# Optimization experiments

Measured on AMD Instinct MI355X. Metric: run time of the kernel, lower is better.

The kernel has to match this reference:

```python
import jax, jax.numpy as jnp
import numpy as np

B, S_IMG, S_TXT, D, H, HD = 1, 4096, 512, 3072, 24, 128
EPS = 1e-5
SCALE = 1.0 / np.sqrt(HD)


def _linear(x, W, b=None):
    # torch nn.Linear: y = x @ W.T + b, W is [out, in]
    y = jnp.einsum('bsd,od->bso', x, W)
    return y if b is None else y + b


def _rmsnorm(x, w):
    # over last dim (head_dim), torch nn.RMSNorm with affine weight
    var = jnp.mean(jnp.square(x), axis=-1, keepdims=True)
    return x * jax.lax.rsqrt(var + EPS) * w


def _rope(x, cos, sin):
    # x: [B, S, H, D]; cos/sin: [S, D]; interleaved-pair rotation
    xr = x.reshape(*x.shape[:-1], HD // 2, 2)
    x_real, x_imag = xr[..., 0], xr[..., 1]
    x_rot = jnp.stack([-x_imag, x_real], axis=-1).reshape(x.shape)
    return x * cos[None, :, None, :] + x_rot * sin[None, :, None, :]


def setup_inputs() -> dict:
    key = jax.random.key(0)
    ks = jax.random.split(key, 24)
    s = 0.02
    inp = {
        'hidden_states': jax.random.normal(ks[0], (B, S_IMG, D), jnp.float32),
        'encoder_hidden_states': jax.random.normal(ks[1], (B, S_TXT, D), jnp.float32),
        'rope_cos': jax.random.uniform(ks[2], (S_IMG + S_TXT, HD), jnp.float32),
        'rope_sin': jax.random.uniform(ks[3], (S_IMG + S_TXT, HD), jnp.float32),
        # image-stream qkv (bias=False)
        'Wq': jax.random.normal(ks[4], (D, D), jnp.float32) * s,
        'Wk': jax.random.normal(ks[5], (D, D), jnp.float32) * s,
        'Wv': jax.random.normal(ks[6], (D, D), jnp.float32) * s,
        # text-stream qkv (bias=True)
        'Waq': jax.random.normal(ks[7], (D, D), jnp.float32) * s,
        'baq': jnp.zeros((D,), jnp.float32),
        'Wak': jax.random.normal(ks[8], (D, D), jnp.float32) * s,
        'bak': jnp.zeros((D,), jnp.float32),
        'Wav': jax.random.normal(ks[9], (D, D), jnp.float32) * s,
        'bav': jnp.zeros((D,), jnp.float32),
        # output projections (bias=True)
        'Wo': jax.random.normal(ks[10], (D, D), jnp.float32) * s,
        'bo': jnp.zeros((D,), jnp.float32),
        'Wao': jax.random.normal(ks[11], (D, D), jnp.float32) * s,
        'bao': jnp.zeros((D,), jnp.float32),
        # RMSNorm weights on head_dim
        'wq_norm': jnp.ones((HD,), jnp.float32),
        'wk_norm': jnp.ones((HD,), jnp.float32),
        'waq_norm': jnp.ones((HD,), jnp.float32),
        'wak_norm': jnp.ones((HD,), jnp.float32),
    }
    return inp


def reference(hidden_states, encoder_hidden_states, rope_cos, rope_sin,
              Wq, Wk, Wv, Waq, baq, Wak, bak, Wav, bav,
              Wo, bo, Wao, bao, wq_norm, wk_norm, waq_norm, wak_norm):
    # image-stream qkv -> [B, S_img, H, HD]
    q = _linear(hidden_states, Wq).reshape(B, S_IMG, H, HD)
    k = _linear(hidden_states, Wk).reshape(B, S_IMG, H, HD)
    v = _linear(hidden_states, Wv).reshape(B, S_IMG, H, HD)
    q = _rmsnorm(q, wq_norm)
    k = _rmsnorm(k, wk_norm)
    # text-stream qkv -> [B, S_txt, H, HD]
    eq = _linear(encoder_hidden_states, Waq, baq).reshape(B, S_TXT, H, HD)
    ek = _linear(encoder_hidden_states, Wak, bak).reshape(B, S_TXT, H, HD)
    ev = _linear(encoder_hidden_states, Wav, bav).reshape(B, S_TXT, H, HD)
    eq = _rmsnorm(eq, waq_norm)
    ek = _rmsnorm(ek, wak_norm)
    # concat [encoder, image] along sequence
    q = jnp.concatenate([eq, q], axis=1)  # [B, S_total, H, HD]
    k = jnp.concatenate([ek, k], axis=1)
    v = jnp.concatenate([ev, v], axis=1)
    # RoPE on joint sequence
    q = _rope(q, rope_cos, rope_sin)
    k = _rope(k, rope_cos, rope_sin)
    # SDPA over joint sequence
    scores = jnp.einsum('bqhd,bkhd->bhqk', q, k) * SCALE
    probs = jax.nn.softmax(scores, axis=-1)
    out = jnp.einsum('bhqk,bkhd->bqhd', probs, v)  # [B, S_total, H, HD]
    out = out.reshape(B, S_IMG + S_TXT, D)
    enc_out = _linear(out[:, :S_TXT], Wao, bao)
    img_out = _linear(out[:, S_TXT:], Wo, bo)
    return (img_out, enc_out)
```

## Files before the change

kernel.cpp:

```cpp
#include <hip/hip_runtime.h>

typedef __bf16 bf16_t;
typedef __bf16 bf16x8 __attribute__((ext_vector_type(8)));
typedef float  f32x4  __attribute__((ext_vector_type(4)));

#define S_IMG 4096
#define S_TXT 512
#define S_TOT 4608
#define DMODEL 3072
#define NH 24
#define HD 128

__device__ __forceinline__ void load_lds16(const void* g, void* l) {
  __builtin_amdgcn_global_load_lds(
      (const __attribute__((address_space(1))) void*)g,
      (__attribute__((address_space(3))) void*)l, 16, 0, 0);
}

#define BARRIER() do { asm volatile("" ::: "memory");                          \
                       __builtin_amdgcn_s_barrier();                           \
                       asm volatile("" ::: "memory"); } while (0)

__global__ __launch_bounds__(256) void f2b_kernel(const float* __restrict__ in,
                                                  bf16_t* __restrict__ out, int n) {
  int i = (blockIdx.x * 256 + threadIdx.x) * 4;
  if (i >= n) return;
  float4 v = *(const float4*)(in + i);
  union { bf16_t b[4]; uint2 u; } pk;
  pk.b[0] = (bf16_t)v.x; pk.b[1] = (bf16_t)v.y;
  pk.b[2] = (bf16_t)v.z; pk.b[3] = (bf16_t)v.w;
  *(uint2*)(out + i) = pk.u;
}

__global__ __launch_bounds__(256) void f2b2_kernel(
    const float* __restrict__ in0, bf16_t* __restrict__ out0,
    const float* __restrict__ in1, bf16_t* __restrict__ out1, int nb) {
  int b = blockIdx.x;
  const float* in = (b < nb) ? in0 : in1;
  bf16_t* out = (b < nb) ? out0 : out1;
  int i = (((b < nb) ? b : b - nb) * 256 + threadIdx.x) * 4;
  float4 v = *(const float4*)(in + i);
  union { bf16_t b[4]; uint2 u; } pk;
  pk.b[0] = (bf16_t)v.x; pk.b[1] = (bf16_t)v.y;
  pk.b[2] = (bf16_t)v.z; pk.b[3] = (bf16_t)v.w;
  *(uint2*)(out + i) = pk.u;
}

template <typename OT>
__global__ __launch_bounds__(512, 2) void gemm256(
    const bf16_t* __restrict__ A0, const bf16_t* __restrict__ B0,
    OT* __restrict__ C0, const float* __restrict__ bias0, int mt0,
    const bf16_t* __restrict__ A1, const bf16_t* __restrict__ B1,
    OT* __restrict__ C1, const float* __restrict__ bias1, int swzq)
{
  const int NT = DMODEL / 64;
  __shared__ bf16_t As[2][2][256 * 32];
  __shared__ bf16_t Bs[2][2][256 * 32];

  int bid = blockIdx.x;
  int t = (bid & 7) * swzq + (bid >> 3);
  int nb0 = mt0 * 12;
  const bf16_t* A; const bf16_t* B; OT* C; const float* bias;
  if (t < nb0) { A = A0; B = B0; C = C0; bias = bias0; }
  else { t -= nb0; A = A1; B = B1; C = C1; bias = bias1; }
  int bx = t % 12, by = t / 12;

  int tid = threadIdx.x;
  int lane = tid & 63, wid = tid >> 6;
  int l15 = lane & 15, lg = lane >> 4;
  int wm = wid >> 2, wn = wid & 3;
  int sx = (lg ^ ((l15 >> 1) & 3)) * 8;

  const bf16_t* Ag = A + (size_t)by * 256 * DMODEL;
  const bf16_t* Bg = B + (size_t)bx * 256 * DMODEL;

  int ur0 = tid >> 2;
  int uc0 = ((tid & 3) ^ ((tid >> 3) & 3)) * 8;

  auto stage = [&](int ht) {
    int T = ht >> 2, sl = ht & 3, kh = sl >> 1;
    const bf16_t* G = (sl & 1) ? Bg : Ag;
    bf16_t* L = (sl & 1) ? &Bs[T & 1][kh][0] : &As[T & 1][kh][0];
    int kbase = T * 64 + kh * 32;
    #pragma unroll
    for (int j = 0; j < 2; j++) {
      int r = j * 128 + ur0;
      load_lds16(G + (size_t)r * DMODEL + kbase + uc0,
                 (char*)L + (size_t)(j * 512 + tid) * 16);
    }
  };

  f32x4 acc[8][4];
  f32x4 zero = {0.f, 0.f, 0.f, 0.f};
  #pragma unroll
  for (int m = 0; m < 8; m++)
    #pragma unroll
    for (int n = 0; n < 4; n++) acc[m][n] = zero;

  stage(0); stage(1); stage(2); stage(3); stage(4); stage(5);
  asm volatile("s_waitcnt vmcnt(8)" ::: "memory");
  BARRIER();

  for (int T = 0; T < NT; ++T) {
    int cur = T & 1;
    const bf16_t* A0s = &As[cur][0][0];
    const bf16_t* A1s = &As[cur][1][0];
    const bf16_t* B0s = &Bs[cur][0][0];
    const bf16_t* B1s = &Bs[cur][1][0];
    bf16x8 af[4], bfr[4];

    #pragma unroll
    for (int n = 0; n < 4; n++)
      bfr[n] = *(const bf16x8*)(B0s + (wn * 64 + n * 16 + l15) * 32 + sx);
    #pragma unroll
    for (int m = 0; m < 4; m++)
      af[m] = *(const bf16x8*)(A0s + (wm * 128 + m * 16 + l15) * 32 + sx);
    if (T + 1 < NT) stage(4 * T + 6);
    BARRIER();
    __builtin_amdgcn_s_setprio(1);
    #pragma unroll
    for (int m = 0; m < 4; m++)
      #pragma unroll
      for (int n = 0; n < 4; n++)
        acc[m][n] = __builtin_amdgcn_mfma_f32_16x16x32_bf16(af[m], bfr[n], acc[m][n], 0, 0, 0);
    __builtin_amdgcn_s_setprio(0);
    BARRIER();

    #pragma unroll
    for (int m = 0; m < 4; m++)
      af[m] = *(const bf16x8*)(A0s + (wm * 128 + 64 + m * 16 + l15) * 32 + sx);
    if (T + 1 < NT) stage(4 * T + 7);
    BARRIER();
    __builtin_amdgcn_s_setprio(1);
    #pragma unroll
    for (int m = 0; m < 4; m++)
      #pragma unroll
      for (int n = 0; n < 4; n++)
        acc[4 + m][n] = __builtin_amdgcn_mfma_f32_16x16x32_bf16(af[m], bfr[n], acc[4 + m][n], 0, 0, 0);
    __builtin_amdgcn_s_setprio(0);
    if (T < NT - 1) asm volatile("s_waitcnt vmcnt(8)" ::: "memory");
    else            asm volatile("s_waitcnt vmcnt(0)" ::: "memory");
    BARRIER();

    #pragma unroll
    for (int n = 0; n < 4; n++)
      bfr[n] = *(const bf16x8*)(B1s + (wn * 64 + n * 16 + l15) * 32 + sx);
    #pragma unroll
    for (int m = 0; m < 4; m++)
      af[m] = *(const bf16x8*)(A1s + (wm * 128 + m * 16 + l15) * 32 + sx);
    if (T + 2 < NT) stage(4 * T + 8);
    BARRIER();
    __builtin_amdgcn_s_setprio(1);
    #pragma unroll
    for (int m = 0; m < 4; m++)
      #pragma unroll
      for (int n = 0; n < 4; n++)
        acc[m][n] = __builtin_amdgcn_mfma_f32_16x16x32_bf16(af[m], bfr[n], acc[m][n], 0, 0, 0);
    __builtin_amdgcn_s_setprio(0);
    BARRIER();

    #pragma unroll
    for (int m = 0; m < 4; m++)
      af[m] = *(const bf16x8*)(A1s + (wm * 128 + 64 + m * 16 + l15) * 32 + sx);
    if (T + 2 < NT) stage(4 * T + 9);
    BARRIER();
    __builtin_amdgcn_s_setprio(1);
    #pragma unroll
    for (int m = 0; m < 4; m++)
      #pragma unroll
      for (int n = 0; n < 4; n++)
        acc[4 + m][n] = __builtin_amdgcn_mfma_f32_16x16x32_bf16(af[m], bfr[n], acc[4 + m][n], 0, 0, 0);
    __builtin_amdgcn_s_setprio(0);
    if (T < NT - 2)       asm volatile("s_waitcnt vmcnt(8)" ::: "memory");
    else if (T == NT - 2) asm volatile("s_waitcnt vmcnt(4)" ::: "memory");
    BARRIER();
  }

  size_t row0 = (size_t)by * 256 + wm * 128;
  int col0 = bx * 256 + wn * 64;
  #pragma unroll
  for (int n = 0; n < 4; n++) {
    int col = col0 + n * 16 + l15;
    float bv = bias ? bias[col] : 0.f;
    #pragma unroll
    for (int m = 0; m < 8; m++) {
      #pragma unroll
      for (int r = 0; r < 4; r++) {
        size_t row = row0 + m * 16 + lg * 4 + r;
        C[row * DMODEL + col] = (OT)(acc[m][n][r] + bv);
      }
    }
  }
}

template <typename OT>
__global__ __launch_bounds__(1024) void gemm1024(
    const bf16_t* __restrict__ A0, const bf16_t* __restrict__ B0,
    OT* __restrict__ C0, const float* __restrict__ bias0, int mt0,
    const bf16_t* __restrict__ A1, const bf16_t* __restrict__ B1,
    OT* __restrict__ C1, const float* __restrict__ bias1, int swzq)
{
  const int NT = DMODEL / 64;
  __shared__ bf16_t As[2][2][256 * 32];
  __shared__ bf16_t Bs[2][2][256 * 32];

  int bid = blockIdx.x;
  int t = (bid & 7) * swzq + (bid >> 3);
  int nb0 = mt0 * 12;
  const bf16_t* A; const bf16_t* B; OT* C; const float* bias;
  if (t < nb0) { A = A0; B = B0; C = C0; bias = bias0; }
  else { t -= nb0; A = A1; B = B1; C = C1; bias = bias1; }
  int bx = t % 12, by = t / 12;

  int tid = threadIdx.x;
  int lane = tid & 63, wid = tid >> 6;
  int l15 = lane & 15, lg = lane >> 4;
  int wm = wid >> 2, wn = wid & 3;
  int sx = (lg ^ ((l15 >> 1) & 3)) * 8;

  const bf16_t* Ag = A + (size_t)by * 256 * DMODEL;
  const bf16_t* Bg = B + (size_t)bx * 256 * DMODEL;

  int ur0 = tid >> 2;
  int uc0 = ((tid & 3) ^ ((tid >> 3) & 3)) * 8;

  auto stage = [&](int ht) {
    int T = ht >> 2, sl = ht & 3, kh = sl >> 1;
    const bf16_t* G = (sl & 1) ? Bg : Ag;
    bf16_t* L = (sl & 1) ? &Bs[T & 1][kh][0] : &As[T & 1][kh][0];
    int kbase = T * 64 + kh * 32;
    load_lds16(G + (size_t)ur0 * DMODEL + kbase + uc0,
               (char*)L + (size_t)tid * 16);
  };

  f32x4 acc[4][4];
  f32x4 zero = {0.f, 0.f, 0.f, 0.f};
  #pragma unroll
  for (int m = 0; m < 4; m++)
    #pragma unroll
    for (int n = 0; n < 4; n++) acc[m][n] = zero;

  stage(0); stage(1); stage(2); stage(3); stage(4); stage(5);
  asm volatile("s_waitcnt vmcnt(4)" ::: "memory");
  BARRIER();

  for (int T = 0; T < NT; ++T) {
    int cur = T & 1;
    bf16x8 af[4], bfr[4];

    {
      const bf16_t* A0s = &As[cur][0][0];
      const bf16_t* B0s = &Bs[cur][0][0];
      #pragma unroll
      for (int n = 0; n < 4; n++)
        bfr[n] = *(const bf16x8*)(B0s + (wn * 64 + n * 16 + l15) * 32 + sx);
      #pragma unroll
      for (int m = 0; m < 4; m++)
        af[m] = *(const bf16x8*)(A0s + (wm * 64 + m * 16 + l15) * 32 + sx);
    }
    if (T + 1 < NT) { stage(4 * T + 6); stage(4 * T + 7); }
    BARRIER();
    __builtin_amdgcn_s_setprio(1);
    #pragma unroll
    for (int m = 0; m < 4; m++)
      #pragma unroll
      for (int n = 0; n < 4; n++)
        acc[m][n] = __builtin_amdgcn_mfma_f32_16x16x32_bf16(af[m], bfr[n], acc[m][n], 0, 0, 0);
    __builtin_amdgcn_s_setprio(0);
    if (T < NT - 1) asm volatile("s_waitcnt vmcnt(4)" ::: "memory");
    else            asm volatile("s_waitcnt vmcnt(0)" ::: "memory");
    BARRIER();

    {
      const bf16_t* A1s = &As[cur][1][0];
      const bf16_t* B1s = &Bs[cur][1][0];
      #pragma unroll
      for (int n = 0; n < 4; n++)
        bfr[n] = *(const bf16x8*)(B1s + (wn * 64 + n * 16 + l15) * 32 + sx);
      #pragma unroll
      for (int m = 0; m < 4; m++)
        af[m] = *(const bf16x8*)(A1s + (wm * 64 + m * 16 + l15) * 32 + sx);
    }
    if (T + 2 < NT) { stage(4 * T + 8); stage(4 * T + 9); }
    BARRIER();
    __builtin_amdgcn_s_setprio(1);
    #pragma unroll
    for (int m = 0; m < 4; m++)
      #pragma unroll
      for (int n = 0; n < 4; n++)
        acc[m][n] = __builtin_amdgcn_mfma_f32_16x16x32_bf16(af[m], bfr[n], acc[m][n], 0, 0, 0);
    __builtin_amdgcn_s_setprio(0);
    if (T < NT - 2)       asm volatile("s_waitcnt vmcnt(4)" ::: "memory");
    else if (T == NT - 2) asm volatile("s_waitcnt vmcnt(2)" ::: "memory");
    BARRIER();
  }

  size_t row0 = (size_t)by * 256 + wm * 64;
  int col0 = bx * 256 + wn * 64;
  #pragma unroll
  for (int n = 0; n < 4; n++) {
    int col = col0 + n * 16 + l15;
    float bv = bias ? bias[col] : 0.f;
    #pragma unroll
    for (int m = 0; m < 4; m++) {
      #pragma unroll
      for (int r = 0; r < 4; r++) {
        size_t row = row0 + m * 16 + lg * 4 + r;
        C[row * DMODEL + col] = (OT)(acc[m][n][r] + bv);
      }
    }
  }
}

__global__ __launch_bounds__(256) void qk_post(
    const bf16_t* __restrict__ qbuf, const bf16_t* __restrict__ kbuf,
    const float* __restrict__ cosb, const float* __restrict__ sinb,
    const float* __restrict__ wqn, const float* __restrict__ wkn,
    const float* __restrict__ waqn, const float* __restrict__ wakn,
    bf16_t* __restrict__ Qh, bf16_t* __restrict__ Kh)
{
  int gw = blockIdx.x * 4 + (threadIdx.x >> 6);
  int lane = threadIdx.x & 63;
  int s = gw / NH, h = gw - (gw / NH) * NH;
  if (s >= S_TOT) return;
  int d0 = lane * 2;
  const bf16_t* qp = qbuf + (size_t)s * DMODEL + h * HD + d0;
  const bf16_t* kp = kbuf + (size_t)s * DMODEL + h * HD + d0;
  float q0 = (float)qp[0], q1 = (float)qp[1];
  float k0 = (float)kp[0], k1 = (float)kp[1];
  float sq = q0 * q0 + q1 * q1, sk = k0 * k0 + k1 * k1;
  #pragma unroll
  for (int m = 1; m < 64; m <<= 1) { sq += __shfl_xor(sq, m); sk += __shfl_xor(sk, m); }
  float rq = rsqrtf(sq * (1.f / HD) + 1e-5f);
  float rk = rsqrtf(sk * (1.f / HD) + 1e-5f);
  const float* qn = (s < S_TXT) ? waqn : wqn;
  const float* kn = (s < S_TXT) ? wakn : wkn;
  q0 *= rq * qn[d0]; q1 *= rq * qn[d0 + 1];
  k0 *= rk * kn[d0]; k1 *= rk * kn[d0 + 1];
  float c0 = cosb[s * HD + d0], c1 = cosb[s * HD + d0 + 1];
  float s0 = sinb[s * HD + d0], s1 = sinb[s * HD + d0 + 1];
  const float SCALE = 0.1275174319942397f;
  float oq0 = (q0 * c0 - q1 * s0) * SCALE;
  float oq1 = (q1 * c1 + q0 * s1) * SCALE;
  float ok0 = k0 * c0 - k1 * s0;
  float ok1 = k1 * c1 + k0 * s1;
  size_t ob = ((size_t)h * S_TOT + s) * HD + d0;
  union { bf16_t b[2]; unsigned int u; } pq, pk;
  pq.b[0] = (bf16_t)oq0; pq.b[1] = (bf16_t)oq1;
  pk.b[0] = (bf16_t)ok0; pk.b[1] = (bf16_t)ok1;
  *(unsigned int*)(Qh + ob) = pq.u;
  *(unsigned int*)(Kh + ob) = pk.u;
}

__global__ __launch_bounds__(256) void v_trans(const bf16_t* __restrict__ vbuf,
                                               bf16_t* __restrict__ Vt) {
  __shared__ bf16_t tile[64 * 130];
  int h = blockIdx.y, s0 = blockIdx.x * 64;
  int tid = threadIdx.x;
  #pragma unroll
  for (int i = 0; i < 16; i++) {
    int idx = tid + i * 256;
    int sr = idx >> 6, dp = idx & 63;
    unsigned int u = *(const unsigned int*)(vbuf + (size_t)(s0 + sr) * DMODEL + h * HD + dp * 2);
    *(unsigned int*)&tile[sr * 130 + dp * 2] = u;
  }
  __syncthreads();
  #pragma unroll
  for (int i = 0; i < 16; i++) {
    int idx = tid + i * 256;
    int d = idx >> 5, scp = idx & 31;
    union { bf16_t b[2]; unsigned int u; } pk;
    pk.b[0] = tile[(scp * 2) * 130 + d];
    pk.b[1] = tile[(scp * 2 + 1) * 130 + d];
    *(unsigned int*)(Vt + ((size_t)h * HD + d) * S_TOT + s0 + scp * 2) = pk.u;
  }
}

__global__ __launch_bounds__(256, 2) void attn_kernel(
    const bf16_t* __restrict__ Qh, const bf16_t* __restrict__ Kh,
    const bf16_t* __restrict__ Vt, bf16_t* __restrict__ O)
{
  int bid = blockIdx.x;
  int orig = (bid & 7) * 108 + (bid >> 3);
  int h = orig / 36;
  int q0 = (orig % 36) * 128;

  int tid = threadIdx.x, w = tid >> 6, lane = tid & 63;
  int l15 = lane & 15, lg = lane >> 4;
  int sw = (l15 & 7) << 4;

  __shared__ bf16_t Ks[2][64 * 128];
  __shared__ bf16_t Vs[2][128 * 64];
  __shared__ bf16_t Ps[4][32 * 64];

  const bf16_t* Kbase = Kh + (size_t)h * S_TOT * HD;
  const bf16_t* Vbase = Vt + (size_t)h * HD * S_TOT;
  bf16_t* Pw = &Ps[w][0];

  bf16x8 qf[2][4];
  #pragma unroll
  for (int qh = 0; qh < 2; qh++) {
    const bf16_t* Qrow = Qh + ((size_t)h * S_TOT + q0 + w * 32 + qh * 16 + l15) * HD + lg * 8;
    #pragma unroll
    for (int dc = 0; dc < 4; dc++) qf[qh][dc] = *(const bf16x8*)(Qrow + dc * 32);
  }

  f32x4 o[2][8];
  f32x4 zero = {0.f, 0.f, 0.f, 0.f};
  #pragma unroll
  for (int qh = 0; qh < 2; qh++)
    #pragma unroll
    for (int i = 0; i < 8; i++) o[qh][i] = zero;
  float m0 = -1e30f, m1 = -1e30f, l0 = 0.f, l1 = 0.f;

#define STAGE(buf, kt) do {                                                    \
    _Pragma("unroll")                                                          \
    for (int i_ = 0; i_ < 4; i_++) {                                           \
      int Lb = (tid + i_ * 256) * 16; int row = Lb >> 8, cb = Lb & 255;        \
      int sb = cb ^ ((row & 7) << 4);                                          \
      load_lds16(Kbase + (size_t)((kt) + row) * HD + (sb >> 1),                \
                 (char*)Ks[buf] + Lb);                                         \
    }                                                                          \
    _Pragma("unroll")                                                          \
    for (int i_ = 0; i_ < 4; i_++) {                                           \
      int Lb = (tid + i_ * 256) * 16; int row = Lb >> 7, cb = Lb & 127;        \
      int sb = cb ^ ((row & 7) << 4);                                          \
      load_lds16(Vbase + (size_t)row * S_TOT + (kt) + (sb >> 1),               \
                 (char*)Vs[buf] + Lb);                                         \
    }                                                                          \
  } while (0)

#define BODY(CUR) do {                                                         \
    f32x4 sacc[2][4];                                                          \
    _Pragma("unroll")                                                          \
    for (int qh = 0; qh < 2; qh++)                                             \
      _Pragma("unroll")                                                        \
      for (int c = 0; c < 4; c++) sacc[qh][c] = zero;                          \
    const char* Kc = (const char*)Ks[CUR];                                     \
    _Pragma("unroll")                                                          \
    for (int c = 0; c < 4; c++) {                                              \
      int row = c * 16 + l15;                                                  \
      int rs = (row & 7) << 4;                                                 \
      const char* kr = Kc + row * 256;                                         \
      _Pragma("unroll")                                                        \
      for (int dc = 0; dc < 4; dc++) {                                         \
        bf16x8 kf = *(const bf16x8*)(kr + ((dc * 64 + lg * 16) ^ rs));         \
        sacc[0][c] = __builtin_amdgcn_mfma_f32_16x16x32_bf16(kf, qf[0][dc], sacc[0][c], 0, 0, 0); \
        sacc[1][c] = __builtin_amdgcn_mfma_f32_16x16x32_bf16(kf, qf[1][dc], sacc[1][c], 0, 0, 0); \
      }                                                                        \
    }                                                                          \
    float px0 = sacc[0][0][0], px1 = sacc[1][0][0];                            \
    _Pragma("unroll")                                                          \
    for (int c = 0; c < 4; c++)                                                \
      _Pragma("unroll")                                                        \
      for (int r = 0; r < 4; r++) {                                            \
        px0 = fmaxf(px0, sacc[0][c][r]);                                       \
        px1 = fmaxf(px1, sacc[1][c][r]);                                       \
      }                                                                        \
    px0 = fmaxf(px0, __shfl_xor(px0, 16)); px0 = fmaxf(px0, __shfl_xor(px0, 32)); \
    px1 = fmaxf(px1, __shfl_xor(px1, 16)); px1 = fmaxf(px1, __shfl_xor(px1, 32)); \
    bool need = (px0 > m0 + 8.f) || (px1 > m1 + 8.f);                          \
    if (__any(need)) {                                                         \
      float mn0 = fmaxf(m0, px0), mn1 = fmaxf(m1, px1);                        \
      float a0 = exp2f(m0 - mn0), a1 = exp2f(m1 - mn1);                        \
      m0 = mn0; m1 = mn1; l0 *= a0; l1 *= a1;                                  \
      _Pragma("unroll")                                                        \
      for (int r = 0; r < 4; r++) {                                            \
        float f0 = __shfl(a0, lg * 4 + r);                                     \
        float f1 = __shfl(a1, lg * 4 + r);                                     \
        _Pragma("unroll")                                                      \
        for (int dn = 0; dn < 8; dn++) { o[0][dn][r] *= f0; o[1][dn][r] *= f1; } \
      }                                                                        \
    }                                                                          \
    _Pragma("unroll")                                                          \
    for (int qh = 0; qh < 2; qh++) {                                           \
      float m = qh ? m1 : m0;                                                  \
      float rsum = 0.f;                                                        \
      char* Prow = (char*)Pw + (qh * 16 + l15) * 128;                          \
      _Pragma("unroll")                                                        \
      for (int c = 0; c < 4; c++) {                                            \
        union { bf16_t b[4]; uint2 u; } pk;                                    \
        _Pragma("unroll")                                                      \
        for (int r = 0; r < 4; r++) {                                          \
          float p = exp2f(sacc[qh][c][r] - m);                                 \
          rsum += p;                                                           \
          pk.b[r] = (bf16_t)p;                                                 \
        }                                                                      \
        *(uint2*)(Prow + ((c * 32 + lg * 8) ^ sw)) = pk.u;                     \
      }                                                                        \
      rsum += __shfl_xor(rsum, 16);                                            \
      rsum += __shfl_xor(rsum, 32);                                            \
      if (qh) l1 += rsum; else l0 += rsum;                                     \
    }                                                                          \
    bf16x8 pf[2][2];                                                           \
    _Pragma("unroll")                                                          \
    for (int qh = 0; qh < 2; qh++) {                                           \
      const char* Prow = (const char*)Pw + (qh * 16 + l15) * 128;              \
      _Pragma("unroll")                                                        \
      for (int kc = 0; kc < 2; kc++)                                           \
        pf[qh][kc] = *(const bf16x8*)(Prow + ((kc * 64 + lg * 16) ^ sw));      \
    }                                                                          \
    const char* Vc = (const char*)Vs[CUR];                                     \
    _Pragma("unroll")                                                          \
    for (int dn = 0; dn < 8; dn++) {                                           \
      int row = dn * 16 + l15;                                                 \
      int rs2 = (row & 7) << 4;                                                \
      const char* vr = Vc + row * 128;                                         \
      bf16x8 vf0 = *(const bf16x8*)(vr + ((lg * 16) ^ rs2));                   \
      bf16x8 vf1 = *(const bf16x8*)(vr + ((64 + lg * 16) ^ rs2));              \
      o[0][dn] = __builtin_amdgcn_mfma_f32_16x16x32_bf16(pf[0][0], vf0, o[0][dn], 0, 0, 0); \
      o[0][dn] = __builtin_amdgcn_mfma_f32_16x16x32_bf16(pf[0][1], vf1, o[0][dn], 0, 0, 0); \
      o[1][dn] = __builtin_amdgcn_mfma_f32_16x16x32_bf16(pf[1][0], vf0, o[1][dn], 0, 0, 0); \
      o[1][dn] = __builtin_amdgcn_mfma_f32_16x16x32_bf16(pf[1][1], vf1, o[1][dn], 0, 0, 0); \
    }                                                                          \
  } while (0)

  STAGE(0, 0);
  __syncthreads();

  const int NT = S_TOT / 64;
  for (int tt = 0; tt < NT; tt += 2) {
    STAGE(1, (tt + 1) * 64);
    BODY(0);
    __syncthreads();
    if (tt + 2 < NT) STAGE(0, (tt + 2) * 64);
    BODY(1);
    __syncthreads();
  }
#undef BODY
#undef STAGE

  #pragma unroll
  for (int qh = 0; qh < 2; qh++) {
    #pragma unroll
    for (int r = 0; r < 4; r++) {
      float lv = __shfl(qh ? l1 : l0, lg * 4 + r);
      float inv = 1.f / lv;
      size_t srow = (size_t)q0 + w * 32 + qh * 16 + lg * 4 + r;
      #pragma unroll
      for (int dn = 0; dn < 8; dn++)
        O[srow * DMODEL + h * HD + dn * 16 + l15] = (bf16_t)(o[qh][dn][r] * inv);
    }
  }
}

extern "C" void kernel_launch(void* const* d_in, const int* in_sizes, int n_in,
                              void* d_out, int out_size, void* d_ws, size_t ws_size,
                              hipStream_t stream) {
  const float* hidden = (const float*)d_in[0];
  const float* enc    = (const float*)d_in[1];
  const float* ropec  = (const float*)d_in[2];
  const float* ropes  = (const float*)d_in[3];
  const float* Wq  = (const float*)d_in[4];
  const float* Wk  = (const float*)d_in[5];
  const float* Wv  = (const float*)d_in[6];
  const float* Waq = (const float*)d_in[7];
  const float* baq = (const float*)d_in[8];
  const float* Wak = (const float*)d_in[9];
  const float* bak = (const float*)d_in[10];
  const float* Wav = (const float*)d_in[11];
  const float* bav = (const float*)d_in[12];
  const float* Wo  = (const float*)d_in[13];
  const float* bo  = (const float*)d_in[14];
  const float* Wao = (const float*)d_in[15];
  const float* bao = (const float*)d_in[16];
  const float* wqn = (const float*)d_in[17];
  const float* wkn = (const float*)d_in[18];
  const float* waqn = (const float*)d_in[19];
  const float* wakn = (const float*)d_in[20];

  const size_t WSZ = (size_t)DMODEL * DMODEL;
  const size_t SEQSZ = (size_t)S_TOT * DMODEL;
  if (ws_size < (2 * WSZ + 6 * SEQSZ) * sizeof(bf16_t)) return;

  bf16_t* s0   = (bf16_t*)d_ws;
  bf16_t* s1   = s0 + WSZ;
  bf16_t* xbi  = s1 + WSZ;
  bf16_t* xbt  = xbi + (size_t)S_IMG * DMODEL;
  bf16_t* qbuf = xbi + SEQSZ;
  bf16_t* kbuf = qbuf + SEQSZ;
  bf16_t* vbuf = kbuf + SEQSZ;
  bf16_t* Kh   = vbuf + SEQSZ;
  bf16_t* Vh   = Kh + SEQSZ;
  bf16_t* Qh   = xbi;
  bf16_t* attn_o = qbuf;
  float* outf = (float*)d_out;

  f2b_kernel<<<S_IMG * DMODEL / 1024, 256, 0, stream>>>(hidden, xbi, S_IMG * DMODEL);
  f2b_kernel<<<S_TXT * DMODEL / 1024, 256, 0, stream>>>(enc, xbt, S_TXT * DMODEL);

  const int WB = (int)(WSZ / 1024);
  f2b2_kernel<<<2 * WB, 256, 0, stream>>>(Wq, s0, Waq, s1, WB);
  gemm1024<bf16_t><<<216, 1024, 0, stream>>>(
      xbi, s0, qbuf + (size_t)S_TXT * DMODEL, nullptr, 16,
      xbt, s1, qbuf, baq, 27);
  f2b2_kernel<<<2 * WB, 256, 0, stream>>>(Wk, s0, Wak, s1, WB);
  gemm256<bf16_t><<<216, 512, 0, stream>>>(
      xbi, s0, kbuf + (size_t)S_TXT * DMODEL, nullptr, 16,
      xbt, s1, kbuf, bak, 27);
  f2b2_kernel<<<2 * WB, 256, 0, stream>>>(Wv, s0, Wav, s1, WB);
  gemm256<bf16_t><<<216, 512, 0, stream>>>(
      xbi, s0, vbuf + (size_t)S_TXT * DMODEL, nullptr, 16,
      xbt, s1, vbuf, bav, 27);

  qk_post<<<S_TOT * NH / 4, 256, 0, stream>>>(qbuf, kbuf, ropec, ropes,
                                              wqn, wkn, waqn, wakn, Qh, Kh);
  v_trans<<<dim3(S_TOT / 64, NH), 256, 0, stream>>>(vbuf, Vh);

  attn_kernel<<<36 * 24, 256, 0, stream>>>(Qh, Kh, Vh, attn_o);

  f2b2_kernel<<<2 * WB, 256, 0, stream>>>(Wo, s0, Wao, s1, WB);
  gemm256<float><<<216, 512, 0, stream>>>(
      attn_o + (size_t)S_TXT * DMODEL, s0, outf, bo, 16,
      attn_o, s1, outf + (size_t)S_IMG * DMODEL, bao, 27);
}
```

Baseline: 938.5 us.

## Fuse V transpose into V-projection GEMM epilogue and use 1024-thread GEMMs

```diff
diff --git a/kernel.cpp b/kernel.cpp
--- a/kernel.cpp
+++ b/kernel.cpp
@@ -47,153 +47,6 @@
 }
 
 template <typename OT>
-__global__ __launch_bounds__(512, 2) void gemm256(
-    const bf16_t* __restrict__ A0, const bf16_t* __restrict__ B0,
-    OT* __restrict__ C0, const float* __restrict__ bias0, int mt0,
-    const bf16_t* __restrict__ A1, const bf16_t* __restrict__ B1,
-    OT* __restrict__ C1, const float* __restrict__ bias1, int swzq)
-{
-  const int NT = DMODEL / 64;
-  __shared__ bf16_t As[2][2][256 * 32];
-  __shared__ bf16_t Bs[2][2][256 * 32];
-
-  int bid = blockIdx.x;
-  int t = (bid & 7) * swzq + (bid >> 3);
-  int nb0 = mt0 * 12;
-  const bf16_t* A; const bf16_t* B; OT* C; const float* bias;
-  if (t < nb0) { A = A0; B = B0; C = C0; bias = bias0; }
-  else { t -= nb0; A = A1; B = B1; C = C1; bias = bias1; }
-  int bx = t % 12, by = t / 12;
-
-  int tid = threadIdx.x;
-  int lane = tid & 63, wid = tid >> 6;
-  int l15 = lane & 15, lg = lane >> 4;
-  int wm = wid >> 2, wn = wid & 3;
-  int sx = (lg ^ ((l15 >> 1) & 3)) * 8;
-
-  const bf16_t* Ag = A + (size_t)by * 256 * DMODEL;
-  const bf16_t* Bg = B + (size_t)bx * 256 * DMODEL;
-
-  int ur0 = tid >> 2;
-  int uc0 = ((tid & 3) ^ ((tid >> 3) & 3)) * 8;
-
-  auto stage = [&](int ht) {
-    int T = ht >> 2, sl = ht & 3, kh = sl >> 1;
-    const bf16_t* G = (sl & 1) ? Bg : Ag;
-    bf16_t* L = (sl & 1) ? &Bs[T & 1][kh][0] : &As[T & 1][kh][0];
-    int kbase = T * 64 + kh * 32;
-    #pragma unroll
-    for (int j = 0; j < 2; j++) {
-      int r = j * 128 + ur0;
-      load_lds16(G + (size_t)r * DMODEL + kbase + uc0,
-                 (char*)L + (size_t)(j * 512 + tid) * 16);
-    }
-  };
-
-  f32x4 acc[8][4];
-  f32x4 zero = {0.f, 0.f, 0.f, 0.f};
-  #pragma unroll
-  for (int m = 0; m < 8; m++)
-    #pragma unroll
-    for (int n = 0; n < 4; n++) acc[m][n] = zero;
-
-  stage(0); stage(1); stage(2); stage(3); stage(4); stage(5);
-  asm volatile("s_waitcnt vmcnt(8)" ::: "memory");
-  BARRIER();
-
-  for (int T = 0; T < NT; ++T) {
-    int cur = T & 1;
-    const bf16_t* A0s = &As[cur][0][0];
-    const bf16_t* A1s = &As[cur][1][0];
-    const bf16_t* B0s = &Bs[cur][0][0];
-    const bf16_t* B1s = &Bs[cur][1][0];
-    bf16x8 af[4], bfr[4];
-
-    #pragma unroll
-    for (int n = 0; n < 4; n++)
-      bfr[n] = *(const bf16x8*)(B0s + (wn * 64 + n * 16 + l15) * 32 + sx);
-    #pragma unroll
-    for (int m = 0; m < 4; m++)
-      af[m] = *(const bf16x8*)(A0s + (wm * 128 + m * 16 + l15) * 32 + sx);
-    if (T + 1 < NT) stage(4 * T + 6);
-    BARRIER();
-    __builtin_amdgcn_s_setprio(1);
-    #pragma unroll
-    for (int m = 0; m < 4; m++)
-      #pragma unroll
-      for (int n = 0; n < 4; n++)
-        acc[m][n] = __builtin_amdgcn_mfma_f32_16x16x32_bf16(af[m], bfr[n], acc[m][n], 0, 0, 0);
-    __builtin_amdgcn_s_setprio(0);
-    BARRIER();
-
-    #pragma unroll
-    for (int m = 0; m < 4; m++)
-      af[m] = *(const bf16x8*)(A0s + (wm * 128 + 64 + m * 16 + l15) * 32 + sx);
-    if (T + 1 < NT) stage(4 * T + 7);
-    BARRIER();
-    __builtin_amdgcn_s_setprio(1);
-    #pragma unroll
-    for (int m = 0; m < 4; m++)
-      #pragma unroll
-      for (int n = 0; n < 4; n++)
-        acc[4 + m][n] = __builtin_amdgcn_mfma_f32_16x16x32_bf16(af[m], bfr[n], acc[4 + m][n], 0, 0, 0);
-    __builtin_amdgcn_s_setprio(0);
-    if (T < NT - 1) asm volatile("s_waitcnt vmcnt(8)" ::: "memory");
-    else            asm volatile("s_waitcnt vmcnt(0)" ::: "memory");
-    BARRIER();
-
-    #pragma unroll
-    for (int n = 0; n < 4; n++)
-      bfr[n] = *(const bf16x8*)(B1s + (wn * 64 + n * 16 + l15) * 32 + sx);
-    #pragma unroll
-    for (int m = 0; m < 4; m++)
-      af[m] = *(const bf16x8*)(A1s + (wm * 128 + m * 16 + l15) * 32 + sx);
-    if (T + 2 < NT) stage(4 * T + 8);
-    BARRIER();
-    __builtin_amdgcn_s_setprio(1);
-    #pragma unroll
-    for (int m = 0; m < 4; m++)
-      #pragma unroll
-      for (int n = 0; n < 4; n++)
-        acc[m][n] = __builtin_amdgcn_mfma_f32_16x16x32_bf16(af[m], bfr[n], acc[m][n], 0, 0, 0);
-    __builtin_amdgcn_s_setprio(0);
-    BARRIER();
-
-    #pragma unroll
-    for (int m = 0; m < 4; m++)
-      af[m] = *(const bf16x8*)(A1s + (wm * 128 + 64 + m * 16 + l15) * 32 + sx);
-    if (T + 2 < NT) stage(4 * T + 9);
-    BARRIER();
-    __builtin_amdgcn_s_setprio(1);
-    #pragma unroll
-    for (int m = 0; m < 4; m++)
-      #pragma unroll
-      for (int n = 0; n < 4; n++)
-        acc[4 + m][n] = __builtin_amdgcn_mfma_f32_16x16x32_bf16(af[m], bfr[n], acc[4 + m][n], 0, 0, 0);
-    __builtin_amdgcn_s_setprio(0);
-    if (T < NT - 2)       asm volatile("s_waitcnt vmcnt(8)" ::: "memory");
-    else if (T == NT - 2) asm volatile("s_waitcnt vmcnt(4)" ::: "memory");
-    BARRIER();
-  }
-
-  size_t row0 = (size_t)by * 256 + wm * 128;
-  int col0 = bx * 256 + wn * 64;
-  #pragma unroll
-  for (int n = 0; n < 4; n++) {
-    int col = col0 + n * 16 + l15;
-    float bv = bias ? bias[col] : 0.f;
-    #pragma unroll
-    for (int m = 0; m < 8; m++) {
-      #pragma unroll
-      for (int r = 0; r < 4; r++) {
-        size_t row = row0 + m * 16 + lg * 4 + r;
-        C[row * DMODEL + col] = (OT)(acc[m][n][r] + bv);
-      }
-    }
-  }
-}
-
-template <typename OT>
 __global__ __launch_bounds__(1024) void gemm1024(
     const bf16_t* __restrict__ A0, const bf16_t* __restrict__ B0,
     OT* __restrict__ C0, const float* __restrict__ bias0, int mt0,
@@ -309,6 +162,141 @@
         C[row * DMODEL + col] = (OT)(acc[m][n][r] + bv);
       }
     }
+  }
+}
+
+__global__ __launch_bounds__(1024) void gemm1024V(
+    const bf16_t* __restrict__ A0, const bf16_t* __restrict__ B0,
+    const float* __restrict__ bias0, int mt0, int soff0,
+    const bf16_t* __restrict__ A1, const bf16_t* __restrict__ B1,
+    const float* __restrict__ bias1, int soff1,
+    bf16_t* __restrict__ Vt, int swzq)
+{
+  const int NT = DMODEL / 64;
+  __shared__ bf16_t As[2][2][256 * 32];
+  __shared__ bf16_t Bs[2][2][256 * 32];
+
+  int bid = blockIdx.x;
+  int t = (bid & 7) * swzq + (bid >> 3);
+  int nb0 = mt0 * 12;
+  const bf16_t* A; const bf16_t* B; const float* bias; int soff;
+  if (t < nb0) { A = A0; B = B0; bias = bias0; soff = soff0; }
+  else { t -= nb0; A = A1; B = B1; bias = bias1; soff = soff1; }
+  int bx = t % 12, by = t / 12;
+
+  int tid = threadIdx.x;
+  int lane = tid & 63, wid = tid >> 6;
+  int l15 = lane & 15, lg = lane >> 4;
+  int wm = wid >> 2, wn = wid & 3;
+  int sx = (lg ^ ((l15 >> 1) & 3)) * 8;
+
+  const bf16_t* Ag = A + (size_t)by * 256 * DMODEL;
+  const bf16_t* Bg = B + (size_t)bx * 256 * DMODEL;
+
+  int ur0 = tid >> 2;
+  int uc0 = ((tid & 3) ^ ((tid >> 3) & 3)) * 8;
+
+  auto stage = [&](int ht) {
+    int T = ht >> 2, sl = ht & 3, kh = sl >> 1;
+    const bf16_t* G = (sl & 1) ? Bg : Ag;
+    bf16_t* L = (sl & 1) ? &Bs[T & 1][kh][0] : &As[T & 1][kh][0];
+    int kbase = T * 64 + kh * 32;
+    load_lds16(G + (size_t)ur0 * DMODEL + kbase + uc0,
+               (char*)L + (size_t)tid * 16);
+  };
+
+  f32x4 acc[4][4];
+  f32x4 zero = {0.f, 0.f, 0.f, 0.f};
+  #pragma unroll
+  for (int m = 0; m < 4; m++)
+    #pragma unroll
+    for (int n = 0; n < 4; n++) acc[m][n] = zero;
+
+  stage(0); stage(1); stage(2); stage(3); stage(4); stage(5);
+  asm volatile("s_waitcnt vmcnt(4)" ::: "memory");
+  BARRIER();
+
+  for (int T = 0; T < NT; ++T) {
+    int cur = T & 1;
+    bf16x8 af[4], bfr[4];
+
+    {
+      const bf16_t* A0s = &As[cur][0][0];
+      const bf16_t* B0s = &Bs[cur][0][0];
+      #pragma unroll
+      for (int n = 0; n < 4; n++)
+        bfr[n] = *(const bf16x8*)(B0s + (wn * 64 + n * 16 + l15) * 32 + sx);
+      #pragma unroll
+      for (int m = 0; m < 4; m++)
+        af[m] = *(const bf16x8*)(A0s + (wm * 64 + m * 16 + l15) * 32 + sx);
+    }
+    if (T + 1 < NT) { stage(4 * T + 6); stage(4 * T + 7); }
+    BARRIER();
+    __builtin_amdgcn_s_setprio(1);
+    #pragma unroll
+    for (int m = 0; m < 4; m++)
+      #pragma unroll
+      for (int n = 0; n < 4; n++)
+        acc[m][n] = __builtin_amdgcn_mfma_f32_16x16x32_bf16(af[m], bfr[n], acc[m][n], 0, 0, 0);
+    __builtin_amdgcn_s_setprio(0);
+    if (T < NT - 1) asm volatile("s_waitcnt vmcnt(4)" ::: "memory");
+    else            asm volatile("s_waitcnt vmcnt(0)" ::: "memory");
+    BARRIER();
+
+    {
+      const bf16_t* A1s = &As[cur][1][0];
+      const bf16_t* B1s = &Bs[cur][1][0];
+      #pragma unroll
+      for (int n = 0; n < 4; n++)
+        bfr[n] = *(const bf16x8*)(B1s + (wn * 64 + n * 16 + l15) * 32 + sx);
+      #pragma unroll
+      for (int m = 0; m < 4; m++)
+        af[m] = *(const bf16x8*)(A1s + (wm * 64 + m * 16 + l15) * 32 + sx);
+    }
+    if (T + 2 < NT) { stage(4 * T + 8); stage(4 * T + 9); }
+    BARRIER();
+    __builtin_amdgcn_s_setprio(1);
+    #pragma unroll
+    for (int m = 0; m < 4; m++)
+      #pragma unroll
+      for (int n = 0; n < 4; n++)
+        acc[m][n] = __builtin_amdgcn_mfma_f32_16x16x32_bf16(af[m], bfr[n], acc[m][n], 0, 0, 0);
+    __builtin_amdgcn_s_setprio(0);
+    if (T < NT - 2)       asm volatile("s_waitcnt vmcnt(4)" ::: "memory");
+    else if (T == NT - 2) asm volatile("s_waitcnt vmcnt(2)" ::: "memory");
+    BARRIER();
+  }
+
+  BARRIER();
+  bf16_t* slab = (wid < 8) ? &As[0][0][0] + (size_t)wid * 4096
+                           : &Bs[0][0][0] + (size_t)(wid - 8) * 4096;
+  int col0 = bx * 256 + wn * 64;
+  #pragma unroll
+  for (int n = 0; n < 4; n++) {
+    int col = n * 16 + l15;
+    float bv = bias ? bias[col0 + col] : 0.f;
+    int msk = (col & 7) << 3;
+    #pragma unroll
+    for (int m = 0; m < 4; m++) {
+      int rowl = m * 16 + lg * 4;
+      union { bf16_t b[4]; unsigned long long ll; } pk;
+      #pragma unroll
+      for (int r = 0; r < 4; r++) pk.b[r] = (bf16_t)(acc[m][n][r] + bv);
+      *(unsigned long long*)&slab[col * 64 + (rowl ^ msk)] = pk.ll;
+    }
+  }
+  asm volatile("s_waitcnt lgkmcnt(0)" ::: "memory");
+  __builtin_amdgcn_sched_barrier(0);
+  int hh = col0 / HD;
+  int dbase = col0 % HD;
+  size_t sbase = (size_t)soff + (size_t)by * 256 + wm * 64;
+  #pragma unroll
+  for (int it = 0; it < 8; it++) {
+    int d = it * 8 + (lane >> 3);
+    int s8 = (lane & 7) * 8;
+    int msk = (d & 7) << 3;
+    bf16x8 v = *(const bf16x8*)&slab[d * 64 + (s8 ^ msk)];
+    *(bf16x8*)(Vt + (size_t)(hh * HD + dbase + d) * S_TOT + sbase + s8) = v;
   }
 }
 
@@ -350,30 +338,6 @@
   pk.b[0] = (bf16_t)ok0; pk.b[1] = (bf16_t)ok1;
   *(unsigned int*)(Qh + ob) = pq.u;
   *(unsigned int*)(Kh + ob) = pk.u;
-}
-
-__global__ __launch_bounds__(256) void v_trans(const bf16_t* __restrict__ vbuf,
-                                               bf16_t* __restrict__ Vt) {
-  __shared__ bf16_t tile[64 * 130];
-  int h = blockIdx.y, s0 = blockIdx.x * 64;
-  int tid = threadIdx.x;
-  #pragma unroll
-  for (int i = 0; i < 16; i++) {
-    int idx = tid + i * 256;
-    int sr = idx >> 6, dp = idx & 63;
-    unsigned int u = *(const unsigned int*)(vbuf + (size_t)(s0 + sr) * DMODEL + h * HD + dp * 2);
-    *(unsigned int*)&tile[sr * 130 + dp * 2] = u;
-  }
-  __syncthreads();
-  #pragma unroll
-  for (int i = 0; i < 16; i++) {
-    int idx = tid + i * 256;
-    int d = idx >> 5, scp = idx & 31;
-    union { bf16_t b[2]; unsigned int u; } pk;
-    pk.b[0] = tile[(scp * 2) * 130 + d];
-    pk.b[1] = tile[(scp * 2 + 1) * 130 + d];
-    *(unsigned int*)(Vt + ((size_t)h * HD + d) * S_TOT + s0 + scp * 2) = pk.u;
-  }
 }
 
 __global__ __launch_bounds__(256, 2) void attn_kernel(
@@ -595,22 +559,21 @@
       xbi, s0, qbuf + (size_t)S_TXT * DMODEL, nullptr, 16,
       xbt, s1, qbuf, baq, 27);
   f2b2_kernel<<<2 * WB, 256, 0, stream>>>(Wk, s0, Wak, s1, WB);
-  gemm256<bf16_t><<<216, 512, 0, stream>>>(
+  gemm1024<bf16_t><<<216, 1024, 0, stream>>>(
       xbi, s0, kbuf + (size_t)S_TXT * DMODEL, nullptr, 16,
       xbt, s1, kbuf, bak, 27);
   f2b2_kernel<<<2 * WB, 256, 0, stream>>>(Wv, s0, Wav, s1, WB);
-  gemm256<bf16_t><<<216, 512, 0, stream>>>(
-      xbi, s0, vbuf + (size_t)S_TXT * DMODEL, nullptr, 16,
-      xbt, s1, vbuf, bav, 27);
+  gemm1024V<<<216, 1024, 0, stream>>>(
+      xbi, s0, nullptr, 16, S_TXT,
+      xbt, s1, bav, 0, Vh, 27);
 
   qk_post<<<S_TOT * NH / 4, 256, 0, stream>>>(qbuf, kbuf, ropec, ropes,
                                               wqn, wkn, waqn, wakn, Qh, Kh);
-  v_trans<<<dim3(S_TOT / 64, NH), 256, 0, stream>>>(vbuf, Vh);
 
   attn_kernel<<<36 * 24, 256, 0, stream>>>(Qh, Kh, Vh, attn_o);
 
   f2b2_kernel<<<2 * WB, 256, 0, stream>>>(Wo, s0, Wao, s1, WB);
-  gemm256<float><<<216, 512, 0, stream>>>(
+  gemm1024<float><<<216, 1024, 0, stream>>>(
       attn_o + (size_t)S_TXT * DMODEL, s0, outf, bo, 16,
       attn_o, s1, outf + (size_t)S_IMG * DMODEL, bao, 27);
 }
```

Result: faster. 837.3 us, median of 3 (-10.8%).
